# Performance work log

Hardware: AMD Instinct MI355X
Metric: run time of the kernel (lower is better)

Reference implementation:

```python
import jax, jax.numpy as jnp
import numpy as np

MORA_DIV = 2


def setup_inputs() -> dict:
    key = jax.random.key(0)
    k1, k2, k3, k4 = jax.random.split(key, 4)
    d = 4096
    m = d // MORA_DIV
    x = jax.random.normal(k1, (4, 2048, d), dtype=jnp.float32)
    weight = jax.random.normal(k2, (d, d), dtype=jnp.float32) * 0.02
    mora = jax.random.normal(k3, (m, m), dtype=jnp.float32) * 0.02
    # dora_mag initialized as column L2 norm of the frozen weight (1, d_in)
    dora_mag = jnp.linalg.norm(weight, axis=0, keepdims=True)
    return {"x": x, "weight": weight, "mora": mora, "dora_mag": dora_mag}


def reference(x, weight, mora, dora_mag):
    # Tile the small adapter into full (d_out, d_in): repeat_interleave on both dims
    adapter = jnp.repeat(jnp.repeat(mora, MORA_DIV, axis=0), MORA_DIV, axis=1)
    w = weight + adapter                      # (d_out, d_in)
    col_norm = jnp.linalg.norm(w, axis=0, keepdims=True)  # (1, d_in)
    w = dora_mag * (w / col_norm)             # DoRA magnitude rescale
    return jnp.einsum('bsd,od->bso', x, w)    # F.linear, no bias
```

## Files before the change

kernel.cpp:

```cpp
#include <hip/hip_runtime.h>
#include <stdint.h>

#define M_TOT 8192
#define N_TOT 4096
#define K_TOT 4096
#define BM 256
#define BN 256
#define BK 64
#define NIT (K_TOT / (2 * BK))

typedef short  s16x8 __attribute__((ext_vector_type(8)));
typedef unsigned short u16x8 __attribute__((ext_vector_type(8)));
typedef float  f32x4 __attribute__((ext_vector_type(4)));

__device__ __forceinline__ unsigned short f32_to_bf16(float f) {
  union { float f; unsigned u; } v; v.f = f;
  unsigned r = v.u + 0x7FFFu + ((v.u >> 16) & 1u);
  return (unsigned short)(r >> 16);
}

__device__ __forceinline__ void gload_lds16(void* lds, const void* g) {
  __builtin_amdgcn_global_load_lds(
      (const __attribute__((address_space(1))) unsigned int*)g,
      (__attribute__((address_space(3))) unsigned int*)lds,
      16, 0, 0);
}

__global__ void colnorm_partial_k(const float* __restrict__ weight,
                                  const float* __restrict__ mora,
                                  float* __restrict__ partials) {
  int d = blockIdx.x * 256 + threadIdx.x;
  int o0 = blockIdx.y * 128;
  float s = 0.f;
  #pragma unroll 4
  for (int o = o0; o < o0 + 128; ++o) {
    float w = weight[(size_t)o * K_TOT + d] + mora[(size_t)(o >> 1) * 2048 + (d >> 1)];
    s = fmaf(w, w, s);
  }
  partials[blockIdx.y * K_TOT + d] = s;
}

__global__ void scale_k(const float* __restrict__ partials,
                        const float* __restrict__ dora_mag,
                        float* __restrict__ scale) {
  int d = blockIdx.x * 256 + threadIdx.x;
  float s = 0.f;
  #pragma unroll
  for (int c = 0; c < 32; ++c) s += partials[c * K_TOT + d];
  scale[d] = dora_mag[d] / sqrtf(s);
}

__global__ void pack_w_k(const float* __restrict__ weight,
                         const float* __restrict__ mora,
                         const float* __restrict__ scale,
                         unsigned short* __restrict__ wb) {
  size_t idx = ((size_t)blockIdx.x * 256 + threadIdx.x) * 8;
  int o = (int)(idx >> 12);
  int d = (int)(idx & (K_TOT - 1));
  float4 w0 = *(const float4*)(weight + idx);
  float4 w1 = *(const float4*)(weight + idx + 4);
  float4 mv = *(const float4*)(mora + (size_t)(o >> 1) * 2048 + (d >> 1));
  float4 s0 = *(const float4*)(scale + d);
  float4 s1 = *(const float4*)(scale + d + 4);
  u16x8 r;
  r[0] = f32_to_bf16((w0.x + mv.x) * s0.x);
  r[1] = f32_to_bf16((w0.y + mv.x) * s0.y);
  r[2] = f32_to_bf16((w0.z + mv.y) * s0.z);
  r[3] = f32_to_bf16((w0.w + mv.y) * s0.w);
  r[4] = f32_to_bf16((w1.x + mv.z) * s1.x);
  r[5] = f32_to_bf16((w1.y + mv.z) * s1.y);
  r[6] = f32_to_bf16((w1.z + mv.w) * s1.z);
  r[7] = f32_to_bf16((w1.w + mv.w) * s1.w);
  *(u16x8*)(wb + idx) = r;
}

__global__ void pack_x_k(const float* __restrict__ x, unsigned short* __restrict__ xb) {
  size_t idx = ((size_t)blockIdx.x * 256 + threadIdx.x) * 8;
  float4 v0 = *(const float4*)(x + idx);
  float4 v1 = *(const float4*)(x + idx + 4);
  u16x8 r;
  r[0] = f32_to_bf16(v0.x); r[1] = f32_to_bf16(v0.y);
  r[2] = f32_to_bf16(v0.z); r[3] = f32_to_bf16(v0.w);
  r[4] = f32_to_bf16(v1.x); r[5] = f32_to_bf16(v1.y);
  r[6] = f32_to_bf16(v1.z); r[7] = f32_to_bf16(v1.w);
  *(u16x8*)(xb + idx) = r;
}

__global__ void __launch_bounds__(512, 2) gemm_bf16_k(
    const unsigned short* __restrict__ xb,
    const unsigned short* __restrict__ wb,
    float* __restrict__ out) {
  __shared__ short lds[2][2][2][128 * 64];

  const int tid = threadIdx.x;
  const int l   = tid & 63;
  const int wid = tid >> 6;
  const int wm  = wid >> 2;
  const int wn  = wid & 3;
  const int wnh = wn >> 1;

  const int orig = blockIdx.x;
  const int swz  = (orig & 7) * (512 >> 3) + (orig >> 3);
  const int by = swz >> 4;
  const int bx = swz & 15;

  const unsigned short* ag = xb + (size_t)(by * BM) * K_TOT;
  const unsigned short* bg = wb + (size_t)(bx * BN) * K_TOT;

  const int row0 = tid >> 3;
  const int kb0  = (tid & 7) ^ (row0 & 7);
  const int off0 = row0 * K_TOT + kb0 * 8;
  const int off1 = off0 + 64 * K_TOT;
  const int ldst = (tid & ~63) * 8;

  const int lrow = l & 15;
  const int lq   = l >> 4;
  const int key  = lrow & 7;
  const int ab0  = lrow * 64 + ((lq) ^ key) * 8;
  const int ab1  = lrow * 64 + ((4 + lq) ^ key) * 8;

  s16x8 aA[4][2], bB[4][2];
  f32x4 acc[8][4] = {};

#define STAGE(buf, op, h, t) { \
    short* d = &lds[buf][op][h][0] + ldst; \
    const unsigned short* s = ((op) ? bg : ag) + (size_t)(h) * 128 * K_TOT + (size_t)(t) * BK; \
    gload_lds16(d, s + off0); \
    gload_lds16(d + 4096, s + off1); }
#define DSA(buf, mh) { const short* p = &lds[buf][0][wm][0]; \
    _Pragma("unroll") for (int mm = 0; mm < 4; ++mm) { \
      aA[mm][0] = *(const s16x8*)(p + ((mh) * 4 + mm) * 1024 + ab0); \
      aA[mm][1] = *(const s16x8*)(p + ((mh) * 4 + mm) * 1024 + ab1); } }
#define DSB(buf, nh) { const short* p = &lds[buf][1][wnh][0] + (wn & 1) * 4096; \
    _Pragma("unroll") for (int nn = 0; nn < 2; ++nn) { \
      bB[(nh) * 2 + nn][0] = *(const s16x8*)(p + ((nh) * 2 + nn) * 1024 + ab0); \
      bB[(nh) * 2 + nn][1] = *(const s16x8*)(p + ((nh) * 2 + nn) * 1024 + ab1); } }
#define MMQ(mh, nh) { __builtin_amdgcn_s_setprio(1); \
    _Pragma("unroll") for (int mm = 0; mm < 4; ++mm) \
      _Pragma("unroll") for (int nn = 0; nn < 2; ++nn) \
        _Pragma("unroll") for (int kh = 0; kh < 2; ++kh) \
          acc[(mh) * 4 + mm][(nh) * 2 + nn] = __builtin_amdgcn_mfma_f32_16x16x32_bf16( \
              aA[mm][kh], bB[(nh) * 2 + nn][kh], acc[(mh) * 4 + mm][(nh) * 2 + nn], 0, 0, 0); \
    __builtin_amdgcn_s_setprio(0); }
#define BARm()  asm volatile("s_barrier" ::: "memory")
#define LGKM0() asm volatile("s_waitcnt lgkmcnt(0)" ::: "memory")
#define VM2()   asm volatile("s_waitcnt vmcnt(2)" ::: "memory")
#define VM0()   asm volatile("s_waitcnt vmcnt(0)" ::: "memory")
#define SB0()   __builtin_amdgcn_sched_barrier(0)

  STAGE(0, 0, 0, 0); STAGE(0, 0, 1, 0); STAGE(0, 1, 0, 0); STAGE(0, 1, 1, 0);
  STAGE(1, 0, 0, 1);
  VM2(); BARm();

  #pragma unroll 1
  for (int i = 0; i < NIT - 1; ++i) {
    const int t1 = 2 * i + 1;
    DSA(0, 0); DSB(0, 0); STAGE(1, 0, 1, t1);
    BARm(); LGKM0(); SB0(); MMQ(0, 0); BARm();
    DSB(0, 1); STAGE(1, 1, 0, t1);
    BARm(); LGKM0(); SB0(); MMQ(0, 1); BARm();
    DSA(0, 1); STAGE(1, 1, 1, t1);
    BARm(); LGKM0(); SB0(); MMQ(1, 0); BARm();
    STAGE(0, 0, 0, t1 + 1);
    BARm(); LGKM0(); SB0(); MMQ(1, 1); VM2(); BARm();
    DSA(1, 0); DSB(1, 0); STAGE(0, 0, 1, t1 + 1);
    BARm(); LGKM0(); SB0(); MMQ(0, 0); BARm();
    DSB(1, 1); STAGE(0, 1, 0, t1 + 1);
    BARm(); LGKM0(); SB0(); MMQ(0, 1); BARm();
    DSA(1, 1); STAGE(0, 1, 1, t1 + 1);
    BARm(); LGKM0(); SB0(); MMQ(1, 0); BARm();
    STAGE(1, 0, 0, t1 + 2);
    BARm(); LGKM0(); SB0(); MMQ(1, 1); VM2(); BARm();
  }

  DSA(0, 0); DSB(0, 0); STAGE(1, 0, 1, 63);
  BARm(); LGKM0(); SB0(); MMQ(0, 0); BARm();
  DSB(0, 1); STAGE(1, 1, 0, 63);
  BARm(); LGKM0(); SB0(); MMQ(0, 1); BARm();
  DSA(0, 1); STAGE(1, 1, 1, 63);
  BARm(); LGKM0(); SB0(); MMQ(1, 0); BARm();
  BARm(); LGKM0(); SB0(); MMQ(1, 1); VM0(); BARm();
  DSA(1, 0); DSB(1, 0);
  BARm(); LGKM0(); SB0(); MMQ(0, 0); BARm();
  DSB(1, 1);
  BARm(); LGKM0(); SB0(); MMQ(0, 1); BARm();
  DSA(1, 1);
  BARm(); LGKM0(); SB0(); MMQ(1, 0); BARm();
  LGKM0(); SB0(); MMQ(1, 1);

#undef STAGE
#undef DSA
#undef DSB
#undef MMQ

  const int row0o = by * BM + wm * 128 + lq * 4;
  const int col0o = bx * BN + wn * 64 + lrow;
  #pragma unroll
  for (int m = 0; m < 8; ++m)
    #pragma unroll
    for (int n = 0; n < 4; ++n) {
      #pragma unroll
      for (int j = 0; j < 4; ++j)
        out[(size_t)(row0o + m * 16 + j) * N_TOT + col0o + n * 16] = acc[m][n][j];
    }
}

__global__ void gemm_fb_k(const float* __restrict__ x, const float* __restrict__ weight,
                          const float* __restrict__ mora, const float* __restrict__ scale,
                          float* __restrict__ out) {
  __shared__ float As[64][17];
  __shared__ float Bs[64][17];
  int t = threadIdx.x;
  int bx = blockIdx.x, by = blockIdx.y;
  int tr = t >> 4, tc = t & 15;
  float c[4][4] = {};
  for (int kt = 0; kt < K_TOT; kt += 16) {
    #pragma unroll
    for (int r = 0; r < 4; ++r) {
      int idx = r * 256 + t;
      int row = idx >> 4, col = idx & 15;
      As[row][col] = x[(size_t)(by * 64 + row) * K_TOT + kt + col];
      int o = bx * 64 + row, d = kt + col;
      Bs[row][col] = (weight[(size_t)o * K_TOT + d] + mora[(size_t)(o >> 1) * 2048 + (d >> 1)]) * scale[d];
    }
    __syncthreads();
    #pragma unroll
    for (int k = 0; k < 16; ++k) {
      float av[4], bv[4];
      #pragma unroll
      for (int i = 0; i < 4; ++i) av[i] = As[tr * 4 + i][k];
      #pragma unroll
      for (int j = 0; j < 4; ++j) bv[j] = Bs[tc * 4 + j][k];
      #pragma unroll
      for (int i = 0; i < 4; ++i)
        #pragma unroll
        for (int j = 0; j < 4; ++j)
          c[i][j] = fmaf(av[i], bv[j], c[i][j]);
    }
    __syncthreads();
  }
  #pragma unroll
  for (int i = 0; i < 4; ++i)
    #pragma unroll
    for (int j = 0; j < 4; ++j)
      out[(size_t)(by * 64 + tr * 4 + i) * N_TOT + bx * 64 + tc * 4 + j] = c[i][j];
}

extern "C" void kernel_launch(void* const* d_in, const int* in_sizes, int n_in,
                              void* d_out, int out_size, void* d_ws, size_t ws_size,
                              hipStream_t stream) {
  const float* x      = (const float*)d_in[0];
  const float* weight = (const float*)d_in[1];
  const float* mora   = (const float*)d_in[2];
  const float* dora   = (const float*)d_in[3];
  float* out = (float*)d_out;

  char* ws = (char*)d_ws;
  float* partials = (float*)ws;
  float* scale    = (float*)(ws + (512 << 10));
  const size_t OFF_W = (size_t)1 << 20;
  unsigned short* wbuf = (unsigned short*)(ws + OFF_W);
  unsigned short* xbuf = (unsigned short*)(ws + OFF_W + (size_t)N_TOT * K_TOT * 2);
  const size_t NEED = OFF_W + (size_t)N_TOT * K_TOT * 2 + (size_t)M_TOT * K_TOT * 2;

  dim3 b256(256);
  colnorm_partial_k<<<dim3(16, 32), b256, 0, stream>>>(weight, mora, partials);
  scale_k<<<16, b256, 0, stream>>>(partials, dora, scale);

  if (ws_size >= NEED) {
    pack_w_k<<<(N_TOT * K_TOT) / (256 * 8), b256, 0, stream>>>(weight, mora, scale, wbuf);
    pack_x_k<<<(M_TOT * K_TOT) / (256 * 8), b256, 0, stream>>>(x, xbuf);
    gemm_bf16_k<<<(M_TOT / BM) * (N_TOT / BN), 512, 0, stream>>>(xbuf, wbuf, out);
  } else {
    gemm_fb_k<<<dim3(N_TOT / 64, M_TOT / 64), b256, 0, stream>>>(x, weight, mora, scale, out);
  }
}
```

Baseline: 307.5 us.

## Prefetch full next K-tile ahead and batch stage loads later in each half

```diff
diff --git a/kernel.cpp b/kernel.cpp
--- a/kernel.cpp
+++ b/kernel.cpp
@@ -144,40 +144,42 @@
     __builtin_amdgcn_s_setprio(0); }
 #define BARm()  asm volatile("s_barrier" ::: "memory")
 #define LGKM0() asm volatile("s_waitcnt lgkmcnt(0)" ::: "memory")
-#define VM2()   asm volatile("s_waitcnt vmcnt(2)" ::: "memory")
+#define VM8()   asm volatile("s_waitcnt vmcnt(8)" ::: "memory")
 #define VM0()   asm volatile("s_waitcnt vmcnt(0)" ::: "memory")
 #define SB0()   __builtin_amdgcn_sched_barrier(0)
 
   STAGE(0, 0, 0, 0); STAGE(0, 0, 1, 0); STAGE(0, 1, 0, 0); STAGE(0, 1, 1, 0);
-  STAGE(1, 0, 0, 1);
-  VM2(); BARm();
+  STAGE(1, 0, 0, 1); STAGE(1, 0, 1, 1); STAGE(1, 1, 0, 1); STAGE(1, 1, 1, 1);
+  VM8(); BARm();
 
   #pragma unroll 1
   for (int i = 0; i < NIT - 1; ++i) {
-    const int t1 = 2 * i + 1;
-    DSA(0, 0); DSB(0, 0); STAGE(1, 0, 1, t1);
+    const int t0 = 2 * i;
+    DSA(0, 0); DSB(0, 0);
     BARm(); LGKM0(); SB0(); MMQ(0, 0); BARm();
-    DSB(0, 1); STAGE(1, 1, 0, t1);
+    DSB(0, 1);
     BARm(); LGKM0(); SB0(); MMQ(0, 1); BARm();
-    DSA(0, 1); STAGE(1, 1, 1, t1);
+    DSA(0, 1);
+    STAGE(0, 1, 0, t0 + 2); STAGE(0, 1, 1, t0 + 2);
     BARm(); LGKM0(); SB0(); MMQ(1, 0); BARm();
-    STAGE(0, 0, 0, t1 + 1);
-    BARm(); LGKM0(); SB0(); MMQ(1, 1); VM2(); BARm();
-    DSA(1, 0); DSB(1, 0); STAGE(0, 0, 1, t1 + 1);
+    STAGE(0, 0, 0, t0 + 2); STAGE(0, 0, 1, t0 + 2);
+    BARm(); LGKM0(); SB0(); MMQ(1, 1); VM8(); BARm();
+    DSA(1, 0); DSB(1, 0);
     BARm(); LGKM0(); SB0(); MMQ(0, 0); BARm();
-    DSB(1, 1); STAGE(0, 1, 0, t1 + 1);
+    DSB(1, 1);
     BARm(); LGKM0(); SB0(); MMQ(0, 1); BARm();
-    DSA(1, 1); STAGE(0, 1, 1, t1 + 1);
+    DSA(1, 1);
+    STAGE(1, 1, 0, t0 + 3); STAGE(1, 1, 1, t0 + 3);
     BARm(); LGKM0(); SB0(); MMQ(1, 0); BARm();
-    STAGE(1, 0, 0, t1 + 2);
-    BARm(); LGKM0(); SB0(); MMQ(1, 1); VM2(); BARm();
-  }
-
-  DSA(0, 0); DSB(0, 0); STAGE(1, 0, 1, 63);
+    STAGE(1, 0, 0, t0 + 3); STAGE(1, 0, 1, t0 + 3);
+    BARm(); LGKM0(); SB0(); MMQ(1, 1); VM8(); BARm();
+  }
+
+  DSA(0, 0); DSB(0, 0);
   BARm(); LGKM0(); SB0(); MMQ(0, 0); BARm();
-  DSB(0, 1); STAGE(1, 1, 0, 63);
+  DSB(0, 1);
   BARm(); LGKM0(); SB0(); MMQ(0, 1); BARm();
-  DSA(0, 1); STAGE(1, 1, 1, 63);
+  DSA(0, 1);
   BARm(); LGKM0(); SB0(); MMQ(1, 0); BARm();
   BARm(); LGKM0(); SB0(); MMQ(1, 1); VM0(); BARm();
   DSA(1, 0); DSB(1, 0);
```

Measured after the change: 314.1 us. 1.02x slower.

## Reschedule K-loop prefetch stages and drop explicit LDS waits and sched barriers

Applied to the files above, without the earlier changes.

```diff
diff --git a/kernel.cpp b/kernel.cpp
--- a/kernel.cpp
+++ b/kernel.cpp
@@ -143,50 +143,51 @@
               aA[mm][kh], bB[(nh) * 2 + nn][kh], acc[(mh) * 4 + mm][(nh) * 2 + nn], 0, 0, 0); \
     __builtin_amdgcn_s_setprio(0); }
 #define BARm()  asm volatile("s_barrier" ::: "memory")
-#define LGKM0() asm volatile("s_waitcnt lgkmcnt(0)" ::: "memory")
-#define VM2()   asm volatile("s_waitcnt vmcnt(2)" ::: "memory")
+#define VM6()   asm volatile("s_waitcnt vmcnt(6)" ::: "memory")
+#define VM4()   asm volatile("s_waitcnt vmcnt(4)" ::: "memory")
 #define VM0()   asm volatile("s_waitcnt vmcnt(0)" ::: "memory")
-#define SB0()   __builtin_amdgcn_sched_barrier(0)
 
   STAGE(0, 0, 0, 0); STAGE(0, 0, 1, 0); STAGE(0, 1, 0, 0); STAGE(0, 1, 1, 0);
-  STAGE(1, 0, 0, 1);
-  VM2(); BARm();
+  STAGE(1, 1, 0, 1); STAGE(1, 1, 1, 1); STAGE(1, 0, 0, 1);
+  VM6(); BARm();
 
   #pragma unroll 1
   for (int i = 0; i < NIT - 1; ++i) {
     const int t1 = 2 * i + 1;
+    const int t2 = t1 + 1;
+    const int t3 = t1 + 2;
     DSA(0, 0); DSB(0, 0); STAGE(1, 0, 1, t1);
-    BARm(); LGKM0(); SB0(); MMQ(0, 0); BARm();
-    DSB(0, 1); STAGE(1, 1, 0, t1);
-    BARm(); LGKM0(); SB0(); MMQ(0, 1); BARm();
-    DSA(0, 1); STAGE(1, 1, 1, t1);
-    BARm(); LGKM0(); SB0(); MMQ(1, 0); BARm();
-    STAGE(0, 0, 0, t1 + 1);
-    BARm(); LGKM0(); SB0(); MMQ(1, 1); VM2(); BARm();
-    DSA(1, 0); DSB(1, 0); STAGE(0, 0, 1, t1 + 1);
-    BARm(); LGKM0(); SB0(); MMQ(0, 0); BARm();
-    DSB(1, 1); STAGE(0, 1, 0, t1 + 1);
-    BARm(); LGKM0(); SB0(); MMQ(0, 1); BARm();
-    DSA(1, 1); STAGE(0, 1, 1, t1 + 1);
-    BARm(); LGKM0(); SB0(); MMQ(1, 0); BARm();
-    STAGE(1, 0, 0, t1 + 2);
-    BARm(); LGKM0(); SB0(); MMQ(1, 1); VM2(); BARm();
+    MMQ(0, 0); BARm();
+    DSB(0, 1);
+    MMQ(0, 1); BARm();
+    DSA(0, 1); STAGE(0, 1, 0, t2);
+    MMQ(1, 0); BARm();
+    STAGE(0, 1, 1, t2);
+    MMQ(1, 1); VM4(); BARm();
+    DSA(1, 0); DSB(1, 0); STAGE(0, 0, 0, t2);
+    MMQ(0, 0); BARm();
+    DSB(1, 1); STAGE(0, 0, 1, t2);
+    MMQ(0, 1); BARm();
+    DSA(1, 1); STAGE(1, 1, 0, t3);
+    MMQ(1, 0); BARm();
+    STAGE(1, 1, 1, t3); STAGE(1, 0, 0, t3);
+    MMQ(1, 1); VM6(); BARm();
   }
 
   DSA(0, 0); DSB(0, 0); STAGE(1, 0, 1, 63);
-  BARm(); LGKM0(); SB0(); MMQ(0, 0); BARm();
-  DSB(0, 1); STAGE(1, 1, 0, 63);
-  BARm(); LGKM0(); SB0(); MMQ(0, 1); BARm();
-  DSA(0, 1); STAGE(1, 1, 1, 63);
-  BARm(); LGKM0(); SB0(); MMQ(1, 0); BARm();
-  BARm(); LGKM0(); SB0(); MMQ(1, 1); VM0(); BARm();
+  MMQ(0, 0); BARm();
+  DSB(0, 1);
+  MMQ(0, 1); BARm();
+  DSA(0, 1);
+  MMQ(1, 0); BARm();
+  MMQ(1, 1); VM0(); BARm();
   DSA(1, 0); DSB(1, 0);
-  BARm(); LGKM0(); SB0(); MMQ(0, 0); BARm();
+  MMQ(0, 0); BARm();
   DSB(1, 1);
-  BARm(); LGKM0(); SB0(); MMQ(0, 1); BARm();
+  MMQ(0, 1); BARm();
   DSA(1, 1);
-  BARm(); LGKM0(); SB0(); MMQ(1, 0); BARm();
-  LGKM0(); SB0(); MMQ(1, 1);
+  MMQ(1, 0); BARm();
+  MMQ(1, 1);
 
 #undef STAGE
 #undef DSA
```

After: 303.1 us. No clear change (-1.5%).
